# Optimization experiments

Hardware: AMD Instinct MI355X
Metric: run time of the kernel (lower is better)

## Reference

```python
import jax, jax.numpy as jnp
import numpy as np

H = W = 4096


def _maxpool3x3(x):
    # 3x3 max pool, stride 1, pad 1 (torch pads with -inf for max pooling)
    return jax.lax.reduce_window(
        x, -jnp.inf, jax.lax.max,
        window_dimensions=(1, 1, 3, 3),
        window_strides=(1, 1, 1, 1),
        padding=[(0, 0), (0, 0), (1, 1), (1, 1)],
    )


def setup_inputs() -> dict:
    key = jax.random.key(0)
    k1, k2 = jax.random.split(key)
    reliability = jax.random.uniform(k1, (1, 1, H, W), dtype=jnp.float32)
    repeatability = jax.random.uniform(k2, (1, 1, H, W), dtype=jnp.float32)
    return {
        "reliability": reliability,
        "repeatability": repeatability,
        "rel_thr": 0.7,
        "rep_thr": 0.7,
    }


def reference(reliability, repeatability, rel_thr, rep_thr):
    # local-maxima detection: a pixel is a maximum iff it equals the 3x3 local max
    mx = _maxpool3x3(repeatability)
    maxima = (repeatability == mx) \
        & (repeatability >= rep_thr) \
        & (reliability >= rel_thr)
    # The original returns maxima.nonzero().t()[2:4] (y,x index compaction),
    # which has a data-dependent shape. The jit-compatible baseline output is
    # the boolean maxima mask [1,1,H,W]; index extraction is a trivial
    # post-processing step (jnp.nonzero(maxima, size=K) outside jit).
    return maxima
```

## Files before the change

### kernel.cpp

```cpp
#include <hip/hip_runtime.h>
#include <hip/hip_bf16.h>
#include <float.h>

#define HH 4096
#define WW 4096
#define RROWS 8

__global__ __launch_bounds__(256) void nms_kernel(
    const float* __restrict__ rel,
    const float* __restrict__ rep,
    const float* __restrict__ rel_thr_p,
    const float* __restrict__ rep_thr_p,
    int* __restrict__ out)
{
    const int x0    = (blockIdx.x * 256 + threadIdx.x) * 4;
    const int ybase = blockIdx.y * RROWS;
    const int lane  = threadIdx.x & 63;

    const float rel_thr = *rel_thr_p;
    const float rep_thr = *rep_thr_p;
    const float NEG = -FLT_MAX;

    auto loadrow = [&](int yy, float4& c) -> float4 {
        float4 h;
        if (yy < 0 || yy >= HH) {
            c = make_float4(NEG, NEG, NEG, NEG);
            return make_float4(NEG, NEG, NEG, NEG);
        }
        const float* row = rep + (size_t)yy * WW;
        const float4 v = *reinterpret_cast<const float4*>(row + x0);
        float left  = __shfl_up(v.w, 1);
        if (lane == 0)  left  = (x0 > 0)      ? row[x0 - 1] : NEG;
        float right = __shfl_down(v.x, 1);
        if (lane == 63) right = (x0 + 4 < WW) ? row[x0 + 4] : NEG;
        c = v;
        h.x = fmaxf(fmaxf(left, v.x), v.y);
        h.y = fmaxf(fmaxf(v.x,  v.y), v.z);
        h.z = fmaxf(fmaxf(v.y,  v.z), v.w);
        h.w = fmaxf(fmaxf(v.z,  v.w), right);
        return h;
    };

    float4 cCur, cNext, cDump;
    float4 hmA = loadrow(ybase - 1, cDump);
    float4 hmB = loadrow(ybase,     cCur);

    #pragma unroll
    for (int i = 0; i < RROWS; ++i) {
        const int y = ybase + i;
        float4 hmC = loadrow(y + 1, cNext);

        const float4 rl = *reinterpret_cast<const float4*>(rel + (size_t)y * WW + x0);

        int4 o;
        float m;
        m   = fmaxf(fmaxf(hmA.x, hmB.x), hmC.x);
        o.x = (cCur.x == m && cCur.x >= rep_thr && rl.x >= rel_thr) ? 1 : 0;
        m   = fmaxf(fmaxf(hmA.y, hmB.y), hmC.y);
        o.y = (cCur.y == m && cCur.y >= rep_thr && rl.y >= rel_thr) ? 1 : 0;
        m   = fmaxf(fmaxf(hmA.z, hmB.z), hmC.z);
        o.z = (cCur.z == m && cCur.z >= rep_thr && rl.z >= rel_thr) ? 1 : 0;
        m   = fmaxf(fmaxf(hmA.w, hmB.w), hmC.w);
        o.w = (cCur.w == m && cCur.w >= rep_thr && rl.w >= rel_thr) ? 1 : 0;

        *reinterpret_cast<int4*>(out + (size_t)y * WW + x0) = o;

        hmA = hmB; hmB = hmC; cCur = cNext;
    }
}

extern "C" void kernel_launch(void* const* d_in, const int* in_sizes, int n_in,
                              void* d_out, int out_size, void* d_ws, size_t ws_size,
                              hipStream_t stream)
{
    const float* rel       = (const float*)d_in[0];
    const float* rep       = (const float*)d_in[1];
    const float* rel_thr_p = (const float*)d_in[2];
    const float* rep_thr_p = (const float*)d_in[3];
    int* out = (int*)d_out;

    dim3 block(256, 1, 1);
    dim3 grid(WW / (256 * 4), HH / RROWS, 1);
    nms_kernel<<<grid, block, 0, stream>>>(rel, rep, rel_thr_p, rep_thr_p, out);
}
```

Before: 35.77 us.

## Remap blocks per XCD and skip reliability loads when no candidate

Flattens the grid and remaps block ids so that consecutive row tiles of the same column strip land on the same XCD, aiming to reuse halo rows in that XCD's L2. Also computes the local-max and repeatability tests first and only loads the reliability row when at least one of the thread's pixels is a candidate. The conditional load adds a branch, and its savings are limited because skipping happens per lane while memory traffic is issued per wavefront.

```diff
diff --git a/kernel.cpp b/kernel.cpp
--- a/kernel.cpp
+++ b/kernel.cpp
@@ -13,8 +13,14 @@
     const float* __restrict__ rep_thr_p,
     int* __restrict__ out)
 {
-    const int x0    = (blockIdx.x * 256 + threadIdx.x) * 4;
-    const int ybase = blockIdx.y * RROWS;
+    const int bid  = blockIdx.x;
+    const int xcd  = bid & 7;
+    const int wgid = xcd * 256 + (bid >> 3);
+    const int bx   = wgid >> 9;
+    const int by   = wgid & 511;
+
+    const int x0    = (bx * 256 + threadIdx.x) * 4;
+    const int ybase = by * RROWS;
     const int lane  = threadIdx.x & 63;
 
     const float rel_thr = *rel_thr_p;
@@ -50,18 +56,24 @@
         const int y = ybase + i;
         float4 hmC = loadrow(y + 1, cNext);
 
-        const float4 rl = *reinterpret_cast<const float4*>(rel + (size_t)y * WW + x0);
+        float m0 = fmaxf(fmaxf(hmA.x, hmB.x), hmC.x);
+        float m1 = fmaxf(fmaxf(hmA.y, hmB.y), hmC.y);
+        float m2 = fmaxf(fmaxf(hmA.z, hmB.z), hmC.z);
+        float m3 = fmaxf(fmaxf(hmA.w, hmB.w), hmC.w);
+        const bool k0 = (cCur.x == m0) && (cCur.x >= rep_thr);
+        const bool k1 = (cCur.y == m1) && (cCur.y >= rep_thr);
+        const bool k2 = (cCur.z == m2) && (cCur.z >= rep_thr);
+        const bool k3 = (cCur.w == m3) && (cCur.w >= rep_thr);
+
+        float4 rl = make_float4(0.f, 0.f, 0.f, 0.f);
+        if (k0 | k1 | k2 | k3)
+            rl = *reinterpret_cast<const float4*>(rel + (size_t)y * WW + x0);
 
         int4 o;
-        float m;
-        m   = fmaxf(fmaxf(hmA.x, hmB.x), hmC.x);
-        o.x = (cCur.x == m && cCur.x >= rep_thr && rl.x >= rel_thr) ? 1 : 0;
-        m   = fmaxf(fmaxf(hmA.y, hmB.y), hmC.y);
-        o.y = (cCur.y == m && cCur.y >= rep_thr && rl.y >= rel_thr) ? 1 : 0;
-        m   = fmaxf(fmaxf(hmA.z, hmB.z), hmC.z);
-        o.z = (cCur.z == m && cCur.z >= rep_thr && rl.z >= rel_thr) ? 1 : 0;
-        m   = fmaxf(fmaxf(hmA.w, hmB.w), hmC.w);
-        o.w = (cCur.w == m && cCur.w >= rep_thr && rl.w >= rel_thr) ? 1 : 0;
+        o.x = (k0 && rl.x >= rel_thr) ? 1 : 0;
+        o.y = (k1 && rl.y >= rel_thr) ? 1 : 0;
+        o.z = (k2 && rl.z >= rel_thr) ? 1 : 0;
+        o.w = (k3 && rl.w >= rel_thr) ? 1 : 0;
 
         *reinterpret_cast<int4*>(out + (size_t)y * WW + x0) = o;
 
@@ -80,6 +92,6 @@
     int* out = (int*)d_out;
 
     dim3 block(256, 1, 1);
-    dim3 grid(WW / (256 * 4), HH / RROWS, 1);
+    dim3 grid(2048, 1, 1);
     nms_kernel<<<grid, block, 0, stream>>>(rel, rep, rel_thr_p, rep_thr_p, out);
 }
```

Measured after the change: 34.74 us. 1.03x faster.
